# Kernel optimization log

Measured on AMD Instinct MI355X. Metric: run time of the kernel, lower is better.

## Reference

```python
import jax, jax.numpy as jnp
import numpy as np

F_FIELDS, HH, WW = 17, 300, 400   # hardcoded cifhr buffer in __init__
H_F, W_F = 38, 50                 # field grid: ~hr_size / stride
STRIDE = 8
V_TH = 0.1
NEIGHBORS = 16
MIN_SCALE = 0.0
FACTOR = 1.0
R = 13                            # window half-width; covers 2*sigma_max = 12 truncation radius


def _approx_exp(x):
    # openpifpaf fast exp approximation; only evaluated for x in [-2, 0]
    y = 1.0 + x / 8.0
    y = y * y
    y = y * y
    y = y * y
    return y


def _accumulate(cifhr, field):
    # field: (F, 5, H_f, W_f) with channels [confidence, x_reg, y_reg, b, scale]
    F = field.shape[0]
    v = field[:, 0]                        # (F,H,W)
    px = field[:, 1] * STRIDE              # hr-grid x position
    py = field[:, 2] * STRIDE              # hr-grid y position
    scale = field[:, 4]
    sigma = jnp.maximum(1.0, 0.5 * scale * STRIDE)
    value = v / NEIGHBORS * FACTOR
    valid = (v >= V_TH) & (scale * STRIDE >= MIN_SCALE)

    cx = jnp.round(px).astype(jnp.int32)
    cy = jnp.round(py).astype(jnp.int32)
    offs = jnp.arange(-R, R + 1, dtype=jnp.int32)   # (K,)
    xx = cx[..., None] + offs                        # (F,H,W,K)
    yy = cy[..., None] + offs                        # (F,H,W,K)
    dx2 = (xx.astype(px.dtype) - px[..., None]) ** 2  # (F,H,W,K)
    dy2 = (yy.astype(py.dtype) - py[..., None]) ** 2  # (F,H,W,K)
    d2 = dy2[..., :, None] + dx2[..., None, :]       # (F,H,W,K,K) y-major
    sigma2 = (sigma ** 2)[..., None, None]
    trunc2 = 4.0 * sigma2                            # truncate = 2*sigma
    inb = ((yy >= 0) & (yy < HH))[..., :, None] & ((xx >= 0) & (xx < WW))[..., None, :]
    mask = (d2 <= trunc2) & inb & valid[..., None, None]
    nearest = (dy2[..., :, None] < 0.25) & (dx2[..., None, :] < 0.25)
    g = jnp.where(nearest, 1.0, _approx_exp(-0.5 * d2 / sigma2))
    contrib = jnp.where(mask, value[..., None, None] * g, 0.0)

    fidx = jnp.arange(F, dtype=jnp.int32)[:, None, None, None, None]
    yc = jnp.clip(yy[..., :, None], 0, HH - 1)
    xc = jnp.clip(xx[..., None, :], 0, WW - 1)
    flat_idx = (fidx * HH + yc) * WW + xc            # (F,H,W,K,K)
    out = cifhr.reshape(-1).at[flat_idx.reshape(-1)].add(contrib.reshape(-1))
    return jnp.minimum(out.reshape(F_FIELDS, HH, WW), 1.0)


def setup_inputs() -> dict:
    key = jax.random.key(0)
    k1, k2, k3, k4, k5 = jax.random.split(key, 5)
    cifhr = jnp.zeros((F_FIELDS, HH, WW), dtype=jnp.float32)
    # confidence in [0,1]
    conf = jax.random.uniform(k1, (F_FIELDS, 1, H_F, W_F), dtype=jnp.float32)
    gx = jnp.broadcast_to(jnp.arange(W_F, dtype=jnp.float32)[None, None, None, :],
                          (F_FIELDS, 1, H_F, W_F))
    gy = jnp.broadcast_to(jnp.arange(H_F, dtype=jnp.float32)[None, None, :, None],
                          (F_FIELDS, 1, H_F, W_F))
    xr = gx + 0.5 * jax.random.normal(k2, (F_FIELDS, 1, H_F, W_F), dtype=jnp.float32)
    yr = gy + 0.5 * jax.random.normal(k3, (F_FIELDS, 1, H_F, W_F), dtype=jnp.float32)
    b = jax.random.uniform(k4, (F_FIELDS, 1, H_F, W_F), dtype=jnp.float32)
    # scale in [0.5, 1.5] -> sigma = max(1, 0.5*scale*stride) <= 6
    scale = 0.5 + jax.random.uniform(k5, (F_FIELDS, 1, H_F, W_F), dtype=jnp.float32)
    x = jnp.concatenate([conf, xr, yr, b, scale], axis=1)  # (17,5,38,50)
    return {"cifhr": cifhr, "x": x}


def reference(cifhr, x):
    return _accumulate(cifhr, x)
```

## Files before the change

kernel.cpp:

```cpp
#include <hip/hip_runtime.h>
#include <hip/hip_bf16.h>
#include <stdint.h>

#define F_FIELDS 17
#define HH 300
#define WW 400
#define H_F 38
#define W_F 50
#define PTS_PER_FIELD (H_F * W_F)
#define RAD 13

#define GX 13
#define GY 10
#define CAP 64

__global__ __launch_bounds__(256) void cifhr_fused_kernel(
    const float* __restrict__ x, const float* __restrict__ cifhr,
    float* __restrict__ out) {
    __shared__ float4 sA[4][CAP];
    __shared__ float  sB[4][CAP];
    __shared__ int    cnt[4];

    const int tid = threadIdx.x;
    const int f = blockIdx.z;
    const int X0 = blockIdx.x * 32;
    const int Y0 = blockIdx.y * 32;
    const int sxmax = min(1, (WW - 1 - X0) >> 4);
    const int symax = min(1, (HH - 1 - Y0) >> 4);
    const int xvhi = X0 + ((sxmax + 1) << 4) - 1;
    const int yvhi = Y0 + ((symax + 1) << 4) - 1;

    if (tid < 4) cnt[tid] = 0;
    __syncthreads();

    const float* base = x + (size_t)(f * 5) * PTS_PER_FIELD;
    for (int p = tid; p < PTS_PER_FIELD; p += 256) {
        float v  = base[p];
        float xr = base[PTS_PER_FIELD + p];
        float yr = base[2 * PTS_PER_FIELD + p];
        float sc = base[4 * PTS_PER_FIELD + p];
        if (!(v >= 0.1f) || !(sc * 8.0f >= 0.0f)) continue;
        float px = xr * 8.0f;
        float py = yr * 8.0f;
        int cx = (int)rintf(px);
        int cy = (int)rintf(py);
        float sigma  = fmaxf(1.0f, 4.0f * sc);
        float sigma2 = sigma * sigma;
        int rp = min(RAD, (int)(2.0f * sigma + 0.5f));
        int xlo = cx - rp, xhi = cx + rp;
        int ylo = cy - rp, yhi = cy + rp;
        if (xhi < X0 || xlo > xvhi || yhi < Y0 || ylo > yvhi) continue;
        int sx0 = max(0, (xlo - X0) >> 4), sx1 = min(sxmax, (xhi - X0) >> 4);
        int sy0 = max(0, (ylo - Y0) >> 4), sy1 = min(symax, (yhi - Y0) >> 4);
        float4 rec = make_float4(px, py, v * 0.0625f, -1.0f / (16.0f * sigma2));
        float tr = 4.0f * sigma2;
        for (int sy = sy0; sy <= sy1; ++sy)
            for (int sx = sx0; sx <= sx1; ++sx) {
                int s = sy * 2 + sx;
                int slot = atomicAdd(&cnt[s], 1);
                if (slot < CAP) { sA[s][slot] = rec; sB[s][slot] = tr; }
            }
    }
    __syncthreads();

    const int lx = tid & 15, lyr = tid >> 4;
    #pragma unroll
    for (int s = 0; s < 4; ++s) {
        int sx = s & 1, sy = s >> 1;
        if (sx > sxmax || sy > symax) continue;
        int xp = X0 + (sx << 4) + lx;
        int yp = Y0 + (sy << 4) + lyr;
        if (yp >= HH) continue;
        int n = min(cnt[s], CAP);
        float xf = (float)xp, yf = (float)yp;
        float acc = 0.0f;
        #pragma unroll 2
        for (int k = 0; k < n; ++k) {
            float4 a = sA[s][k];
            float tr = sB[s][k];
            float dx  = xf - a.x;
            float dy  = yf - a.y;
            float dx2 = dx * dx;
            float dy2 = dy * dy;
            float d2  = dy2 + dx2;
            float t8 = fmaf(a.w, d2, 1.0f);
            t8 = t8 * t8; t8 = t8 * t8; t8 = t8 * t8;
            float g = (dy2 < 0.25f && dx2 < 0.25f) ? 1.0f : t8;
            acc += (d2 <= tr) ? a.z * g : 0.0f;
        }
        size_t idx = ((size_t)f * HH + yp) * WW + xp;
        out[idx] = fminf(acc + cifhr[idx], 1.0f);
    }
}

extern "C" void kernel_launch(void* const* d_in, const int* in_sizes, int n_in,
                              void* d_out, int out_size, void* d_ws, size_t ws_size,
                              hipStream_t stream) {
    const float* cifhr = (const float*)d_in[0];
    const float* x     = (const float*)d_in[1];
    float* out = (float*)d_out;

    dim3 grid(GX, GY, F_FIELDS);
    cifhr_fused_kernel<<<grid, 256, 0, stream>>>(x, cifhr, out);
}
```

Measured before the change: 81.84 us.

## Assign one wavefront per subtile with 2x2 pixels per thread

Each 64-lane wavefront now owns one 16x16 subtile, and every thread accumulates a 2x2 pixel patch. This replaces the loop in which each thread walked all four subtiles. A shared-memory record loaded once is reused across four pixels, and the dx/dy squares are shared, which cuts LDS traffic and per-pixel arithmetic. Stores become float2 vectors. The record cap rises from 64 to 80, which lowers the risk of dropping contributions but uses more shared memory. Empty subtiles now exit their wave early.

```diff
diff --git a/kernel.cpp b/kernel.cpp
--- a/kernel.cpp
+++ b/kernel.cpp
@@ -12,7 +12,7 @@
 
 #define GX 13
 #define GY 10
-#define CAP 64
+#define CAP 80
 
 __global__ __launch_bounds__(256) void cifhr_fused_kernel(
     const float* __restrict__ x, const float* __restrict__ cifhr,
@@ -63,33 +63,66 @@
     }
     __syncthreads();
 
-    const int lx = tid & 15, lyr = tid >> 4;
-    #pragma unroll
-    for (int s = 0; s < 4; ++s) {
-        int sx = s & 1, sy = s >> 1;
-        if (sx > sxmax || sy > symax) continue;
-        int xp = X0 + (sx << 4) + lx;
-        int yp = Y0 + (sy << 4) + lyr;
-        if (yp >= HH) continue;
-        int n = min(cnt[s], CAP);
-        float xf = (float)xp, yf = (float)yp;
-        float acc = 0.0f;
-        #pragma unroll 2
-        for (int k = 0; k < n; ++k) {
-            float4 a = sA[s][k];
-            float tr = sB[s][k];
-            float dx  = xf - a.x;
-            float dy  = yf - a.y;
-            float dx2 = dx * dx;
-            float dy2 = dy * dy;
-            float d2  = dy2 + dx2;
-            float t8 = fmaf(a.w, d2, 1.0f);
-            t8 = t8 * t8; t8 = t8 * t8; t8 = t8 * t8;
-            float g = (dy2 < 0.25f && dx2 < 0.25f) ? 1.0f : t8;
-            acc += (d2 <= tr) ? a.z * g : 0.0f;
+    const int s  = tid >> 6;
+    const int ln = tid & 63;
+    const int sx = s & 1, sy = s >> 1;
+    if (sx > sxmax || sy > symax) return;
+
+    const int xb = X0 + (sx << 4) + ((ln & 7) << 1);
+    const int yb = Y0 + (sy << 4) + ((ln >> 3) << 1);
+    const float xf0 = (float)xb,  xf1 = (float)(xb + 1);
+    const float yf0 = (float)yb,  yf1 = (float)(yb + 1);
+
+    const int n = min(cnt[s], CAP);
+    float a00 = 0.0f, a01 = 0.0f, a10 = 0.0f, a11 = 0.0f;
+    for (int k = 0; k < n; ++k) {
+        float4 a = sA[s][k];
+        float tr = sB[s][k];
+        float dx0 = xf0 - a.x, dx1 = xf1 - a.x;
+        float dy0 = yf0 - a.y, dy1 = yf1 - a.y;
+        float dx0s = dx0 * dx0, dx1s = dx1 * dx1;
+        float dy0s = dy0 * dy0, dy1s = dy1 * dy1;
+        {
+            float d2 = dy0s + dx0s;
+            float t8 = fmaf(a.w, d2, 1.0f); t8 *= t8; t8 *= t8; t8 *= t8;
+            float g  = (fmaxf(dy0s, dx0s) < 0.25f) ? 1.0f : t8;
+            a00 += (d2 <= tr) ? a.z * g : 0.0f;
         }
-        size_t idx = ((size_t)f * HH + yp) * WW + xp;
-        out[idx] = fminf(acc + cifhr[idx], 1.0f);
+        {
+            float d2 = dy0s + dx1s;
+            float t8 = fmaf(a.w, d2, 1.0f); t8 *= t8; t8 *= t8; t8 *= t8;
+            float g  = (fmaxf(dy0s, dx1s) < 0.25f) ? 1.0f : t8;
+            a01 += (d2 <= tr) ? a.z * g : 0.0f;
+        }
+        {
+            float d2 = dy1s + dx0s;
+            float t8 = fmaf(a.w, d2, 1.0f); t8 *= t8; t8 *= t8; t8 *= t8;
+            float g  = (fmaxf(dy1s, dx0s) < 0.25f) ? 1.0f : t8;
+            a10 += (d2 <= tr) ? a.z * g : 0.0f;
+        }
+        {
+            float d2 = dy1s + dx1s;
+            float t8 = fmaf(a.w, d2, 1.0f); t8 *= t8; t8 *= t8; t8 *= t8;
+            float g  = (fmaxf(dy1s, dx1s) < 0.25f) ? 1.0f : t8;
+            a11 += (d2 <= tr) ? a.z * g : 0.0f;
+        }
+    }
+
+    if (yb < HH) {
+        size_t idx = ((size_t)f * HH + yb) * WW + xb;
+        const float2 c = *(const float2*)(cifhr + idx);
+        float2 o;
+        o.x = fminf(a00 + c.x, 1.0f);
+        o.y = fminf(a01 + c.y, 1.0f);
+        *(float2*)(out + idx) = o;
+    }
+    if (yb + 1 < HH) {
+        size_t idx = ((size_t)f * HH + yb + 1) * WW + xb;
+        const float2 c = *(const float2*)(cifhr + idx);
+        float2 o;
+        o.x = fminf(a10 + c.x, 1.0f);
+        o.y = fminf(a11 + c.y, 1.0f);
+        *(float2*)(out + idx) = o;
     }
 }
 
```

Measured after the change: 79.71 us. -2.6%, faster.
